# Optimization experiments

Hardware: AMD Instinct MI355X
Metric: run time of the kernel (lower is better)

## Reference

```python
import jax, jax.numpy as jnp
import numpy as np

V, E, H = 1024, 32, 64
D = 8                     # number of tree levels (root at depth 0)
PER = 149796              # nodes per non-root level
N = 1 + 7 * PER           # 1048573 total nodes


def setup_inputs() -> dict:
    rng = np.random.default_rng(0)
    sizes = [1] + [PER] * (D - 1)
    off = np.concatenate([[0], np.cumsum(sizes)])
    depth = np.repeat(np.arange(D), sizes).astype(np.int64)
    parent = np.zeros(N, dtype=np.int64)  # root points to itself (harmless: its h is 0 when read)
    for l in range(1, D):
        parent[off[l]:off[l + 1]] = rng.integers(off[l - 1], off[l], sizes[l])
    token_ids = rng.integers(0, V, N).astype(np.int64)

    key = jax.random.key(0)
    ks = jax.random.split(key, 7)
    s = 0.05
    return {
        "token_ids": jnp.asarray(token_ids),
        "parent": jnp.asarray(parent),
        "depth": jnp.asarray(depth),
        "max_depth": D - 1,
        "emb": jax.random.normal(ks[0], (V, E), jnp.float32) * s,
        "W_iou_w": jax.random.normal(ks[1], (3 * H, E), jnp.float32) * s,
        "W_iou_b": jax.random.normal(ks[2], (3 * H,), jnp.float32) * s,
        "U_iou_w": jax.random.normal(ks[3], (3 * H, H), jnp.float32) * s,
        "W_f_w": jax.random.normal(ks[4], (H, E), jnp.float32) * s,
        "W_f_b": jax.random.normal(ks[5], (H,), jnp.float32) * s,
        "U_f_w": jax.random.normal(ks[6], (H, H), jnp.float32) * s,
    }


def reference(token_ids, parent, depth, max_depth, emb,
              W_iou_w, W_iou_b, U_iou_w, W_f_w, W_f_b, U_f_w):
    n = token_ids.shape[0]
    hid = U_f_w.shape[0]
    x = emb[token_ids]                                 # [N, E]
    wiou_x = x @ W_iou_w.T + W_iou_b                   # [N, 3H] (input part, precomputed)
    wf_x = x @ W_f_w.T + W_f_b                         # [N, H]
    h = jnp.zeros((n, hid), x.dtype)
    c = jnp.zeros((n, hid), x.dtype)
    # level-synchronous bottom-up sweep (deepest level first); children of a
    # depth-d node are exactly at depth d+1, already finalized when d is processed
    for d in range(max_depth, -1, -1):
        h_sum = jax.ops.segment_sum(h, parent, num_segments=n)        # child-sum per parent
        f = jax.nn.sigmoid(wf_x[parent] + h @ U_f_w.T)                # forget gate per child edge
        fc = jax.ops.segment_sum(f * c, parent, num_segments=n)      # sum_k f_k * c_k per parent
        iou = wiou_x + h_sum @ U_iou_w.T
        i, o, u = jnp.split(iou, 3, axis=-1)
        c_new = jax.nn.sigmoid(i) * jnp.tanh(u) + fc
        h_new = jax.nn.sigmoid(o) * jnp.tanh(c_new)
        m = (depth == d)[:, None]
        h = jnp.where(m, h_new, h)
        c = jnp.where(m, c_new, c)
    return h[0]  # root hidden state, matching TreeLSTMEncoder.forward
```

## Files before the change

kernel.cpp:

```cpp
#include <hip/hip_runtime.h>

#define PER  149796
#define NN   1048573
#define HDIM 64
#define EDIM 32
#define NIOU 192
#define STG  96

typedef _Float16 f16;
typedef _Float16 f16x8 __attribute__((ext_vector_type(8)));
typedef _Float16 f16x4 __attribute__((ext_vector_type(4)));
typedef _Float16 f16x2 __attribute__((ext_vector_type(2)));
typedef float    f32x4 __attribute__((ext_vector_type(4)));

typedef __attribute__((address_space(1))) const unsigned gu32;
typedef __attribute__((address_space(3))) unsigned lu32;

__device__ __forceinline__ float sigf(float x){ return 1.0f/(1.0f+__expf(-x)); }
__device__ __forceinline__ float tanh_f(float x){
  float ax = fabsf(x);
  float e  = __expf(-2.0f*ax);
  float t  = (1.0f - e)/(1.0f + e);
  return x < 0.0f ? -t : t;
}

__global__ __launch_bounds__(256) void countAll_kernel(const int* __restrict__ parent,
                                                       int* __restrict__ cnt){
  int idx = blockIdx.x*256 + threadIdx.x;
  if (idx >= 6*PER) return;
  atomicAdd(&cnt[parent[1 + PER + idx]], 1);
}

__global__ __launch_bounds__(256) void scan1_kernel(const int* __restrict__ cnt, int* __restrict__ bsum){
  __shared__ int sc[256];
  int b = blockIdx.x, t = threadIdx.x;
  int base = b*1024 + t*4;
  int s = 0;
  #pragma unroll
  for (int e=0;e<4;e++){ int idx=base+e; if (idx<NN) s += cnt[idx]; }
  sc[t]=s; __syncthreads();
  for (int d=128; d>0; d>>=1){ if (t<d) sc[t]+=sc[t+d]; __syncthreads(); }
  if (t==0) bsum[b]=sc[0];
}

__global__ __launch_bounds__(1024) void scan2_kernel(const int* __restrict__ bsum, int* __restrict__ bbase){
  __shared__ int sc[1024];
  int t=threadIdx.x;
  sc[t]=bsum[t]; __syncthreads();
  for (int d=1; d<1024; d<<=1){
    int v = (t>=d)? sc[t-d] : 0; __syncthreads();
    sc[t]+=v; __syncthreads();
  }
  bbase[t] = (t==0)?0:sc[t-1];
}

__global__ __launch_bounds__(256) void scan3_kernel(const int* __restrict__ cnt, const int* __restrict__ bbase,
                                                    int* __restrict__ off, int* __restrict__ cursor){
  __shared__ int sc[256];
  int b=blockIdx.x, t=threadIdx.x;
  int base=b*1024+t*4;
  int e0 = (base  <NN)?cnt[base  ]:0;
  int e1 = (base+1<NN)?cnt[base+1]:0;
  int e2 = (base+2<NN)?cnt[base+2]:0;
  int e3 = (base+3<NN)?cnt[base+3]:0;
  int tsum=e0+e1+e2+e3;
  sc[t]=tsum; __syncthreads();
  for (int d=1; d<256; d<<=1){
    int v=(t>=d)?sc[t-d]:0; __syncthreads();
    sc[t]+=v; __syncthreads();
  }
  int x = bbase[b] + ((t==0)?0:sc[t-1]);
  if (base  <NN){ off[base  ]=x;          cursor[base  ]=x; }
  if (base+1<NN){ off[base+1]=x+e0;       cursor[base+1]=x+e0; }
  if (base+2<NN){ off[base+2]=x+e0+e1;    cursor[base+2]=x+e0+e1; }
  if (base+3<NN){ off[base+3]=x+e0+e1+e2; cursor[base+3]=x+e0+e1+e2; }
}

__global__ __launch_bounds__(256) void scatterAll_kernel(const int* __restrict__ parent,
    int* __restrict__ cursor, int* __restrict__ childrow){
  int idx = blockIdx.x*256 + threadIdx.x;
  if (idx >= 6*PER) return;
  int g = 1 + PER + idx;
  int jp = parent[g];
  int pos = atomicAdd(&cursor[jp], 1);
  childrow[pos] = idx % PER;
}

__global__ __launch_bounds__(256) void tablepack_kernel(
    const float* __restrict__ emb, const float* __restrict__ Wiou, const float* __restrict__ biou,
    const float* __restrict__ Wf, const float* __restrict__ bf,
    const float* __restrict__ Uf, const float* __restrict__ Uiou,
    float* __restrict__ embWiou, float* __restrict__ embWf,
    f16* __restrict__ Bfp, f16* __restrict__ Biop)
{
  if (blockIdx.x < 1024){
    int v = blockIdx.x;
    int m = threadIdx.x;
    const float* x = emb + (size_t)v*EDIM;
    if (m < NIOU){
      float a = biou[m];
      #pragma unroll
      for (int e=0;e<EDIM;e++) a += Wiou[m*EDIM+e]*x[e];
      embWiou[(size_t)v*NIOU + m] = a;
    } else {
      int mm = m - NIOU;
      float a = bf[mm];
      #pragma unroll
      for (int e=0;e<EDIM;e++) a += Wf[mm*EDIM+e]*x[e];
      embWf[(size_t)v*HDIM + mm] = a;
    }
  } else {
    for (int i = threadIdx.x; i < 2*4*64*8; i += 256){
      int j = i & 7, L = (i>>3)&63, st = i>>9;
      int t = st & 3, s = st >> 2;
      int k = s*32 + (L>>4)*8 + j;
      int n = t*16 + (L&15);
      Bfp[i] = (f16)Uf[n*HDIM + k];
    }
    for (int i = threadIdx.x; i < 2*12*64*8; i += 256){
      int j = i & 7, L = (i>>3)&63, st = i>>9;
      int t = st % 12, s = st / 12;
      int k = s*32 + (L>>4)*8 + j;
      int n = t*16 + (L&15);
      Biop[i] = (f16)Uiou[n*HDIM + k];
    }
  }
}

__global__ __launch_bounds__(256) void node_fused(
    const int* __restrict__ tok, const int* __restrict__ parent,
    const int* __restrict__ off, const int* __restrict__ childrow,
    const float* __restrict__ embWiou, const float* __restrict__ embWf,
    const f16* __restrict__ Biopack, const f16* __restrict__ Ufpack,
    const f16x2* __restrict__ HFin, f16x2* __restrict__ HFout,
    int poff, int leafLevel)
{
  __shared__ __align__(16) char smem[STG*HDIM*4];
  f16x2* stage = (f16x2*)smem;
  f16*   Ah    = (f16*)smem;
  f16*   FAf   = (f16*)(smem + 9216);
  int lane = threadIdx.x & 63;
  int wv   = __builtin_amdgcn_readfirstlane(threadIdx.x >> 6);
  int p0   = wv*16;
  int j0b  = blockIdx.x*64;
  int j0   = j0b + p0;

  float hs[16], fa[16];
  #pragma unroll
  for (int i=0;i<16;i++){ hs[i]=0.f; fa[i]=0.f; }

  if (!leafLevel){
    int ei = j0b + 64; if (ei > PER) ei = PER;
    int S = off[poff + j0b];
    int E = off[poff + ei];
    int sB[17];
    #pragma unroll
    for (int i=0;i<=16;i++){
      int jj = j0 + i; if (jj > PER) jj = PER;
      sB[i] = off[poff + jj];
    }
    const unsigned* HFinU = (const unsigned*)HFin;
    for (int cb = S; cb < E; cb += STG){
      int n = E - cb; if (n > STG) n = STG;
      for (int r = wv; r < n; r += 4){
        int srow = childrow[cb + r];
        gu32* gp = (gu32*)(HFinU + (size_t)srow*HDIM) + lane;
        __builtin_amdgcn_global_load_lds(gp, (lu32*)&stage[r*HDIM], 4, 0, 0);
      }
      __syncthreads();
      int lim = cb + n;
      #pragma unroll
      for (int i=0;i<16;i++){
        int lo = sB[i]   > cb  ? sB[i]   : cb;
        int hi = sB[i+1] < lim ? sB[i+1] : lim;
        for (int p=lo; p<hi; ++p){
          f16x2 v = stage[(p-cb)*HDIM + lane];
          hs[i] += (float)v.x; fa[i] += (float)v.y;
        }
      }
      __syncthreads();
    }
  }
  #pragma unroll
  for (int i=0;i<16;i++){
    Ah[(p0+i)*72 + lane]  = (f16)hs[i];
    FAf[(p0+i)*68 + lane] = (f16)fa[i];
  }
  __syncthreads();
  int q = lane>>4, c16 = lane&15;
  f16x8 A0 = *(const f16x8*)(Ah + (p0+c16)*72 + q*8);
  f16x8 A1 = *(const f16x8*)(Ah + (p0+c16)*72 + 32 + q*8);
  const f16x8* Bp = (const f16x8*)Biopack;
  f32x4 acc[12];
  #pragma unroll
  for (int nt=0;nt<12;nt++) acc[nt] = (f32x4){0.f,0.f,0.f,0.f};
  #pragma unroll
  for (int nt=0;nt<12;nt++){
    f16x8 B0 = Bp[nt*64 + lane];
    f16x8 B1 = Bp[(12+nt)*64 + lane];
    acc[nt] = __builtin_amdgcn_mfma_f32_16x16x32_f16(A0, B0, acc[nt], 0,0,0);
    acc[nt] = __builtin_amdgcn_mfma_f32_16x16x32_f16(A1, B1, acc[nt], 0,0,0);
  }
  float cc[4][4];
  f16   hh[4][4];
  int   wt_[4]; bool ok_[4];
  #pragma unroll
  for (int r=0;r<4;r++){
    int j = j0 + q*4 + r;
    bool ok = j < PER;
    int jl = ok ? j : PER-1;
    int g = poff + jl;
    int tk = tok[g];
    const float* tr = embWiou + (size_t)tk*NIOU;
    wt_[r] = tok[parent[g]];
    ok_[r] = ok;
    int prow = p0 + q*4 + r;
    #pragma unroll
    for (int nt=0;nt<4;nt++){
      int col = nt*16 + c16;
      float ai = acc[nt][r]   + tr[col];
      float ao = acc[nt+4][r] + tr[64+col];
      float au = acc[nt+8][r] + tr[128+col];
      float fav = (float)FAf[prow*68 + col];
      float c = sigf(ai)*tanh_f(au) + fav;
      float h = sigf(ao)*tanh_f(c);
      cc[r][nt] = c;
      hh[r][nt] = (f16)h;
    }
  }
  __syncthreads();
  #pragma unroll
  for (int r=0;r<4;r++)
    #pragma unroll
    for (int nt=0;nt<4;nt++)
      Ah[(p0+q*4+r)*72 + nt*16 + c16] = hh[r][nt];
  __syncthreads();
  f16x8 H0 = *(const f16x8*)(Ah + (p0+c16)*72 + q*8);
  f16x8 H1 = *(const f16x8*)(Ah + (p0+c16)*72 + 32 + q*8);
  const f16x8* Up = (const f16x8*)Ufpack;
  f32x4 g4[4];
  #pragma unroll
  for (int nt=0;nt<4;nt++) g4[nt] = (f32x4){0.f,0.f,0.f,0.f};
  #pragma unroll
  for (int nt=0;nt<4;nt++){
    f16x8 B0 = Up[nt*64 + lane];
    f16x8 B1 = Up[(4+nt)*64 + lane];
    g4[nt] = __builtin_amdgcn_mfma_f32_16x16x32_f16(H0, B0, g4[nt], 0,0,0);
    g4[nt] = __builtin_amdgcn_mfma_f32_16x16x32_f16(H1, B1, g4[nt], 0,0,0);
  }
  #pragma unroll
  for (int r=0;r<4;r++){
    if (!ok_[r]) continue;
    const float* wr = embWf + (size_t)wt_[r]*HDIM;
    int j = j0 + q*4 + r;
    #pragma unroll
    for (int nt=0;nt<4;nt++){
      int col = nt*16 + c16;
      float v = sigf(g4[nt][r] + wr[col]) * cc[r][nt];
      f16x2 o; o.x = hh[r][nt]; o.y = (f16)v;
      HFout[(size_t)j*HDIM + col] = o;
    }
  }
}

__global__ __launch_bounds__(256) void rootred_kernel(
    const f16x2* __restrict__ HFin, float* __restrict__ rootacc)
{
  int t = blockIdx.x*blockDim.x + threadIdx.x;
  int m = t & 63;
  int j0 = t >> 6;
  int jstep = (gridDim.x*blockDim.x) >> 6;
  float af=0.f, ah=0.f;
  for (int j=j0; j<PER; j+=jstep){
    f16x2 v = HFin[(size_t)j*HDIM + m];
    ah += (float)v.x;
    af += (float)v.y;
  }
  __shared__ float red[256];
  red[threadIdx.x]=af; __syncthreads();
  if (threadIdx.x < 64) atomicAdd(&rootacc[m],    red[m]+red[64+m]+red[128+m]+red[192+m]);
  __syncthreads();
  red[threadIdx.x]=ah; __syncthreads();
  if (threadIdx.x < 64) atomicAdd(&rootacc[64+m], red[m]+red[64+m]+red[128+m]+red[192+m]);
}

__global__ void rootnode_kernel(
    const int* __restrict__ tok, const float* __restrict__ emb,
    const float* __restrict__ Wiou, const float* __restrict__ biou, const float* __restrict__ Uiou,
    const float* __restrict__ rootacc, float* __restrict__ out)
{
  int m = threadIdx.x;
  if (m >= HDIM) return;
  int t = tok[0];
  float ai=biou[m], ao=biou[HDIM+m], au=biou[2*HDIM+m];
  for (int e=0;e<EDIM;e++){
    float xe = emb[(size_t)t*EDIM+e];
    ai += Wiou[(size_t)m*EDIM+e]*xe;
    ao += Wiou[(size_t)(HDIM+m)*EDIM+e]*xe;
    au += Wiou[(size_t)(2*HDIM+m)*EDIM+e]*xe;
  }
  for (int k=0;k<HDIM;k++){
    float hv = rootacc[64+k];
    ai += Uiou[(size_t)m*HDIM+k]*hv;
    ao += Uiou[(size_t)(HDIM+m)*HDIM+k]*hv;
    au += Uiou[(size_t)(2*HDIM+m)*HDIM+k]*hv;
  }
  float c = sigf(ai)*tanh_f(au) + rootacc[m];
  out[m] = sigf(ao)*tanh_f(c);
}

static inline char* alignup(char* p){
  uintptr_t u = (uintptr_t)p;
  u = (u + 255) & ~(uintptr_t)255;
  return (char*)u;
}

extern "C" void kernel_launch(void* const* d_in, const int* in_sizes, int n_in,
                              void* d_out, int out_size, void* d_ws, size_t ws_size,
                              hipStream_t stream)
{
  const int*   tok    = (const int*)d_in[0];
  const int*   parent = (const int*)d_in[1];
  const float* emb    = (const float*)d_in[4];
  const float* Wiou   = (const float*)d_in[5];
  const float* biou   = (const float*)d_in[6];
  const float* Uiou   = (const float*)d_in[7];
  const float* Wf     = (const float*)d_in[8];
  const float* bf     = (const float*)d_in[9];
  const float* Uf     = (const float*)d_in[10];
  float* out = (float*)d_out;

  char* w = (char*)d_ws;
  f16x2* HFA     = (f16x2*)w;  w = alignup(w + (size_t)PER*HDIM*sizeof(f16x2));
  f16x2* HFB     = (f16x2*)w;  w = alignup(w + (size_t)PER*HDIM*sizeof(f16x2));
  int*   cnt     = (int*)w;    w = alignup(w + (size_t)NN*sizeof(int));
  int*   off     = (int*)w;    w = alignup(w + (size_t)NN*sizeof(int));
  int*   cursor  = (int*)w;    w = alignup(w + (size_t)NN*sizeof(int));
  int*   childrow= (int*)w;    w = alignup(w + ((size_t)6*PER + 256)*sizeof(int));
  int*   bsum    = (int*)w;    w = alignup(w + 1024*sizeof(int));
  int*   bbase   = (int*)w;    w = alignup(w + 1024*sizeof(int));
  float* embWiou = (float*)w;  w = alignup(w + 1024*NIOU*sizeof(float));
  float* embWf   = (float*)w;  w = alignup(w + 1024*HDIM*sizeof(float));
  float* rootacc = (float*)w;  w = alignup(w + 128*sizeof(float));
  f16*   Ufpack  = (f16*)w;    w = alignup(w + 2*4*64*8*sizeof(f16));
  f16*   Biopack = (f16*)w;    w = alignup(w + 2*12*64*8*sizeof(f16));

  const int gALL = (6*PER + 255)/256;

  hipMemsetAsync(cnt, 0, (size_t)(1 + 6*PER)*sizeof(int), stream);
  hipMemsetAsync(rootacc, 0, 128*sizeof(float), stream);

  countAll_kernel  <<<gALL, 256, 0, stream>>>(parent, cnt);
  scan1_kernel     <<<1024, 256, 0, stream>>>(cnt, bsum);
  scan2_kernel     <<<1, 1024, 0, stream>>>(bsum, bbase);
  scan3_kernel     <<<1024, 256, 0, stream>>>(cnt, bbase, off, cursor);
  scatterAll_kernel<<<gALL, 256, 0, stream>>>(parent, cursor, childrow);
  tablepack_kernel <<<1025, 256, 0, stream>>>(emb, Wiou, biou, Wf, bf, Uf, Uiou,
                                              embWiou, embWf, Ufpack, Biopack);

  f16x2* bufs[2] = {HFA, HFB};
  int outIdx = 0;
  f16x2* last = HFA;
  for (int d=7; d>=1; --d){
    int poff = 1 + (d-1)*PER;
    f16x2* in  = bufs[1-outIdx];
    f16x2* ou  = bufs[outIdx];
    node_fused<<<(PER + 63)/64, 256, 0, stream>>>(tok, parent, off, childrow,
                                                  embWiou, embWf, Biopack, Ufpack,
                                                  in, ou, poff, (d==7) ? 1 : 0);
    last = ou;
    outIdx ^= 1;
  }

  rootred_kernel<<<256, 256, 0, stream>>>(last, rootacc);
  rootnode_kernel<<<1, 64, 0, stream>>>(tok, emb, Wiou, biou, Uiou, rootacc, out);
}
```

Before: 553.6 us.

## Replace CSR child gather with packed-fp16 atomic scatter into parent accumulators

Drops the count/scan/scatter CSR build and the per-level child gather. Each node now adds its h and f*c contributions into its parent's row with global fp16x2 atomics, and the next level reads that row directly. Blocks shrink to one wave of 16 nodes. This removes the preprocessing kernels and the indirect gathers, but adds a memset per level, heavy atomic traffic, and fp16 accumulation whose rounding depends on atomic order.

```diff
diff --git a/kernel.cpp b/kernel.cpp
--- a/kernel.cpp
+++ b/kernel.cpp
@@ -1,20 +1,17 @@
 #include <hip/hip_runtime.h>
+#include <hip/hip_fp16.h>
+#include <string.h>
 
 #define PER  149796
 #define NN   1048573
 #define HDIM 64
 #define EDIM 32
 #define NIOU 192
-#define STG  96
 
 typedef _Float16 f16;
 typedef _Float16 f16x8 __attribute__((ext_vector_type(8)));
-typedef _Float16 f16x4 __attribute__((ext_vector_type(4)));
 typedef _Float16 f16x2 __attribute__((ext_vector_type(2)));
 typedef float    f32x4 __attribute__((ext_vector_type(4)));
-
-typedef __attribute__((address_space(1))) const unsigned gu32;
-typedef __attribute__((address_space(3))) unsigned lu32;
 
 __device__ __forceinline__ float sigf(float x){ return 1.0f/(1.0f+__expf(-x)); }
 __device__ __forceinline__ float tanh_f(float x){
@@ -24,66 +21,15 @@
   return x < 0.0f ? -t : t;
 }
 
-__global__ __launch_bounds__(256) void countAll_kernel(const int* __restrict__ parent,
-                                                       int* __restrict__ cnt){
-  int idx = blockIdx.x*256 + threadIdx.x;
-  if (idx >= 6*PER) return;
-  atomicAdd(&cnt[parent[1 + PER + idx]], 1);
-}
-
-__global__ __launch_bounds__(256) void scan1_kernel(const int* __restrict__ cnt, int* __restrict__ bsum){
-  __shared__ int sc[256];
-  int b = blockIdx.x, t = threadIdx.x;
-  int base = b*1024 + t*4;
-  int s = 0;
-  #pragma unroll
-  for (int e=0;e<4;e++){ int idx=base+e; if (idx<NN) s += cnt[idx]; }
-  sc[t]=s; __syncthreads();
-  for (int d=128; d>0; d>>=1){ if (t<d) sc[t]+=sc[t+d]; __syncthreads(); }
-  if (t==0) bsum[b]=sc[0];
-}
-
-__global__ __launch_bounds__(1024) void scan2_kernel(const int* __restrict__ bsum, int* __restrict__ bbase){
-  __shared__ int sc[1024];
-  int t=threadIdx.x;
-  sc[t]=bsum[t]; __syncthreads();
-  for (int d=1; d<1024; d<<=1){
-    int v = (t>=d)? sc[t-d] : 0; __syncthreads();
-    sc[t]+=v; __syncthreads();
-  }
-  bbase[t] = (t==0)?0:sc[t-1];
-}
-
-__global__ __launch_bounds__(256) void scan3_kernel(const int* __restrict__ cnt, const int* __restrict__ bbase,
-                                                    int* __restrict__ off, int* __restrict__ cursor){
-  __shared__ int sc[256];
-  int b=blockIdx.x, t=threadIdx.x;
-  int base=b*1024+t*4;
-  int e0 = (base  <NN)?cnt[base  ]:0;
-  int e1 = (base+1<NN)?cnt[base+1]:0;
-  int e2 = (base+2<NN)?cnt[base+2]:0;
-  int e3 = (base+3<NN)?cnt[base+3]:0;
-  int tsum=e0+e1+e2+e3;
-  sc[t]=tsum; __syncthreads();
-  for (int d=1; d<256; d<<=1){
-    int v=(t>=d)?sc[t-d]:0; __syncthreads();
-    sc[t]+=v; __syncthreads();
-  }
-  int x = bbase[b] + ((t==0)?0:sc[t-1]);
-  if (base  <NN){ off[base  ]=x;          cursor[base  ]=x; }
-  if (base+1<NN){ off[base+1]=x+e0;       cursor[base+1]=x+e0; }
-  if (base+2<NN){ off[base+2]=x+e0+e1;    cursor[base+2]=x+e0+e1; }
-  if (base+3<NN){ off[base+3]=x+e0+e1+e2; cursor[base+3]=x+e0+e1+e2; }
-}
-
-__global__ __launch_bounds__(256) void scatterAll_kernel(const int* __restrict__ parent,
-    int* __restrict__ cursor, int* __restrict__ childrow){
-  int idx = blockIdx.x*256 + threadIdx.x;
-  if (idx >= 6*PER) return;
-  int g = 1 + PER + idx;
-  int jp = parent[g];
-  int pos = atomicAdd(&cursor[jp], 1);
-  childrow[pos] = idx % PER;
+__device__ __forceinline__ void atomAddH2(f16x2* p, f16 a, f16 b){
+#if defined(__HIP_DEVICE_COMPILE__)
+  typedef _Float16 h2 __attribute__((ext_vector_type(2)));
+  h2 v; v[0]=a; v[1]=b;
+  (void)__builtin_amdgcn_global_atomic_fadd_v2f16(
+      (__attribute__((address_space(1))) h2*)p, v);
+#else
+  (void)p; (void)a; (void)b;
+#endif
 }
 
 __global__ __launch_bounds__(256) void tablepack_kernel(
@@ -127,69 +73,38 @@
   }
 }
 
-__global__ __launch_bounds__(256) void node_fused(
+__global__ __launch_bounds__(64,4) void level_kernel(
     const int* __restrict__ tok, const int* __restrict__ parent,
-    const int* __restrict__ off, const int* __restrict__ childrow,
     const float* __restrict__ embWiou, const float* __restrict__ embWf,
     const f16* __restrict__ Biopack, const f16* __restrict__ Ufpack,
-    const f16x2* __restrict__ HFin, f16x2* __restrict__ HFout,
-    int poff, int leafLevel)
-{
-  __shared__ __align__(16) char smem[STG*HDIM*4];
-  f16x2* stage = (f16x2*)smem;
-  f16*   Ah    = (f16*)smem;
-  f16*   FAf   = (f16*)(smem + 9216);
-  int lane = threadIdx.x & 63;
-  int wv   = __builtin_amdgcn_readfirstlane(threadIdx.x >> 6);
-  int p0   = wv*16;
-  int j0b  = blockIdx.x*64;
-  int j0   = j0b + p0;
-
-  float hs[16], fa[16];
-  #pragma unroll
-  for (int i=0;i<16;i++){ hs[i]=0.f; fa[i]=0.f; }
-
-  if (!leafLevel){
-    int ei = j0b + 64; if (ei > PER) ei = PER;
-    int S = off[poff + j0b];
-    int E = off[poff + ei];
-    int sB[17];
-    #pragma unroll
-    for (int i=0;i<=16;i++){
-      int jj = j0 + i; if (jj > PER) jj = PER;
-      sB[i] = off[poff + jj];
-    }
-    const unsigned* HFinU = (const unsigned*)HFin;
-    for (int cb = S; cb < E; cb += STG){
-      int n = E - cb; if (n > STG) n = STG;
-      for (int r = wv; r < n; r += 4){
-        int srow = childrow[cb + r];
-        gu32* gp = (gu32*)(HFinU + (size_t)srow*HDIM) + lane;
-        __builtin_amdgcn_global_load_lds(gp, (lu32*)&stage[r*HDIM], 4, 0, 0);
-      }
-      __syncthreads();
-      int lim = cb + n;
-      #pragma unroll
-      for (int i=0;i<16;i++){
-        int lo = sB[i]   > cb  ? sB[i]   : cb;
-        int hi = sB[i+1] < lim ? sB[i+1] : lim;
-        for (int p=lo; p<hi; ++p){
-          f16x2 v = stage[(p-cb)*HDIM + lane];
-          hs[i] += (float)v.x; fa[i] += (float)v.y;
-        }
-      }
-      __syncthreads();
-    }
-  }
-  #pragma unroll
-  for (int i=0;i<16;i++){
-    Ah[(p0+i)*72 + lane]  = (f16)hs[i];
-    FAf[(p0+i)*68 + lane] = (f16)fa[i];
-  }
-  __syncthreads();
+    const f16x2* __restrict__ accIn, f16x2* __restrict__ accOut,
+    int poff, int ppoff, int mode)
+{
+  __shared__ f16 Ah[16*72];
+  __shared__ f16 FAf[16*68];
+  int lane = threadIdx.x;
+  int j0   = blockIdx.x*16;
   int q = lane>>4, c16 = lane&15;
-  f16x8 A0 = *(const f16x8*)(Ah + (p0+c16)*72 + q*8);
-  f16x8 A1 = *(const f16x8*)(Ah + (p0+c16)*72 + 32 + q*8);
+
+  if (mode != 0){
+    #pragma unroll
+    for (int i=0;i<16;i++){
+      int j = j0 + i; if (j > PER-1) j = PER-1;
+      f16x2 v = accIn[(size_t)j*HDIM + lane];
+      Ah[i*72 + lane]  = v.x;
+      FAf[i*68 + lane] = v.y;
+    }
+  } else {
+    #pragma unroll
+    for (int i=0;i<16;i++){
+      Ah[i*72 + lane]  = (f16)0.f;
+      FAf[i*68 + lane] = (f16)0.f;
+    }
+  }
+  __syncthreads();
+  f16x8 A0 = *(const f16x8*)(Ah + c16*72 + q*8);
+  f16x8 A1 = *(const f16x8*)(Ah + c16*72 + 32 + q*8);
+
   const f16x8* Bp = (const f16x8*)Biopack;
   f32x4 acc[12];
   #pragma unroll
@@ -203,7 +118,7 @@
   }
   float cc[4][4];
   f16   hh[4][4];
-  int   wt_[4]; bool ok_[4];
+  int   prow_[4]; int wt_[4]; bool ok_[4];
   #pragma unroll
   for (int r=0;r<4;r++){
     int j = j0 + q*4 + r;
@@ -212,9 +127,16 @@
     int g = poff + jl;
     int tk = tok[g];
     const float* tr = embWiou + (size_t)tk*NIOU;
-    wt_[r] = tok[parent[g]];
     ok_[r] = ok;
-    int prow = p0 + q*4 + r;
+    if (mode != 2){
+      int pg = parent[g];
+      prow_[r] = pg - ppoff;
+      wt_[r]   = tok[pg];
+    } else {
+      prow_[r] = jl;
+      wt_[r]   = tok[0];
+    }
+    int prow = q*4 + r;
     #pragma unroll
     for (int nt=0;nt<4;nt++){
       int col = nt*16 + c16;
@@ -233,10 +155,10 @@
   for (int r=0;r<4;r++)
     #pragma unroll
     for (int nt=0;nt<4;nt++)
-      Ah[(p0+q*4+r)*72 + nt*16 + c16] = hh[r][nt];
-  __syncthreads();
-  f16x8 H0 = *(const f16x8*)(Ah + (p0+c16)*72 + q*8);
-  f16x8 H1 = *(const f16x8*)(Ah + (p0+c16)*72 + 32 + q*8);
+      Ah[(q*4+r)*72 + nt*16 + c16] = hh[r][nt];
+  __syncthreads();
+  f16x8 H0 = *(const f16x8*)(Ah + c16*72 + q*8);
+  f16x8 H1 = *(const f16x8*)(Ah + c16*72 + 32 + q*8);
   const f16x8* Up = (const f16x8*)Ufpack;
   f32x4 g4[4];
   #pragma unroll
@@ -252,13 +174,17 @@
   for (int r=0;r<4;r++){
     if (!ok_[r]) continue;
     const float* wr = embWf + (size_t)wt_[r]*HDIM;
-    int j = j0 + q*4 + r;
+    size_t rb = (size_t)prow_[r]*HDIM;
     #pragma unroll
     for (int nt=0;nt<4;nt++){
       int col = nt*16 + c16;
       float v = sigf(g4[nt][r] + wr[col]) * cc[r][nt];
-      f16x2 o; o.x = hh[r][nt]; o.y = (f16)v;
-      HFout[(size_t)j*HDIM + col] = o;
+      if (mode == 2){
+        f16x2 o; o.x = hh[r][nt]; o.y = (f16)v;
+        accOut[rb + col] = o;
+      } else {
+        atomAddH2(&accOut[rb + col], hh[r][nt], (f16)v);
+      }
     }
   }
 }
@@ -331,47 +257,36 @@
   float* out = (float*)d_out;
 
   char* w = (char*)d_ws;
-  f16x2* HFA     = (f16x2*)w;  w = alignup(w + (size_t)PER*HDIM*sizeof(f16x2));
-  f16x2* HFB     = (f16x2*)w;  w = alignup(w + (size_t)PER*HDIM*sizeof(f16x2));
-  int*   cnt     = (int*)w;    w = alignup(w + (size_t)NN*sizeof(int));
-  int*   off     = (int*)w;    w = alignup(w + (size_t)NN*sizeof(int));
-  int*   cursor  = (int*)w;    w = alignup(w + (size_t)NN*sizeof(int));
-  int*   childrow= (int*)w;    w = alignup(w + ((size_t)6*PER + 256)*sizeof(int));
-  int*   bsum    = (int*)w;    w = alignup(w + 1024*sizeof(int));
-  int*   bbase   = (int*)w;    w = alignup(w + 1024*sizeof(int));
+  size_t BUF = (size_t)PER*HDIM*sizeof(f16x2);
+  f16x2* bufA    = (f16x2*)w;  w = alignup(w + BUF);
+  f16x2* bufB    = (f16x2*)w;  w = alignup(w + BUF);
   float* embWiou = (float*)w;  w = alignup(w + 1024*NIOU*sizeof(float));
   float* embWf   = (float*)w;  w = alignup(w + 1024*HDIM*sizeof(float));
   float* rootacc = (float*)w;  w = alignup(w + 128*sizeof(float));
   f16*   Ufpack  = (f16*)w;    w = alignup(w + 2*4*64*8*sizeof(f16));
   f16*   Biopack = (f16*)w;    w = alignup(w + 2*12*64*8*sizeof(f16));
 
-  const int gALL = (6*PER + 255)/256;
-
-  hipMemsetAsync(cnt, 0, (size_t)(1 + 6*PER)*sizeof(int), stream);
-  hipMemsetAsync(rootacc, 0, 128*sizeof(float), stream);
-
-  countAll_kernel  <<<gALL, 256, 0, stream>>>(parent, cnt);
-  scan1_kernel     <<<1024, 256, 0, stream>>>(cnt, bsum);
-  scan2_kernel     <<<1, 1024, 0, stream>>>(bsum, bbase);
-  scan3_kernel     <<<1024, 256, 0, stream>>>(cnt, bbase, off, cursor);
-  scatterAll_kernel<<<gALL, 256, 0, stream>>>(parent, cursor, childrow);
-  tablepack_kernel <<<1025, 256, 0, stream>>>(emb, Wiou, biou, Wf, bf, Uf, Uiou,
-                                              embWiou, embWf, Ufpack, Biopack);
-
-  f16x2* bufs[2] = {HFA, HFB};
-  int outIdx = 0;
-  f16x2* last = HFA;
-  for (int d=7; d>=1; --d){
-    int poff = 1 + (d-1)*PER;
-    f16x2* in  = bufs[1-outIdx];
-    f16x2* ou  = bufs[outIdx];
-    node_fused<<<(PER + 63)/64, 256, 0, stream>>>(tok, parent, off, childrow,
-                                                  embWiou, embWf, Biopack, Ufpack,
-                                                  in, ou, poff, (d==7) ? 1 : 0);
-    last = ou;
-    outIdx ^= 1;
-  }
-
-  rootred_kernel<<<256, 256, 0, stream>>>(last, rootacc);
+  const int NB = (PER + 15)/16;
+
+  (void)hipMemsetAsync(rootacc, 0, 128*sizeof(float), stream);
+  tablepack_kernel<<<1025, 256, 0, stream>>>(emb, Wiou, biou, Wf, bf, Uf, Uiou,
+                                             embWiou, embWf, Ufpack, Biopack);
+
+  f16x2* accIn  = nullptr;
+  f16x2* accOut = bufA;
+  (void)hipMemsetAsync(bufA, 0, BUF, stream);
+  level_kernel<<<NB, 64, 0, stream>>>(tok, parent, embWiou, embWf, Biopack, Ufpack,
+                                      nullptr, bufA, 1 + 6*PER, 1 + 5*PER, 0);
+  accIn = bufA; accOut = bufB;
+  for (int d=6; d>=2; --d){
+    (void)hipMemsetAsync(accOut, 0, BUF, stream);
+    level_kernel<<<NB, 64, 0, stream>>>(tok, parent, embWiou, embWf, Biopack, Ufpack,
+                                        accIn, accOut, 1 + (d-1)*PER, 1 + (d-2)*PER, 1);
+    f16x2* t2 = accIn; accIn = accOut; accOut = t2;
+  }
+  level_kernel<<<NB, 64, 0, stream>>>(tok, parent, embWiou, embWf, Biopack, Ufpack,
+                                      accIn, accOut, 1, 0, 2);
+
+  rootred_kernel<<<256, 256, 0, stream>>>(accOut, rootacc);
   rootnode_kernel<<<1, 64, 0, stream>>>(tok, emb, Wiou, biou, Uiou, rootacc, out);
 }
```

Result: no change. 546.6 us (-1.3%).
